# Optimization experiments

Hardware: AMD Instinct MI355X
Metric: run time of the kernel (lower is better)

Reference implementation:

```python
import jax, jax.numpy as jnp
import numpy as np
import math

HEADS = 8
HID = 32
MODES = 8
IN_CH = 4
SEQ = 32
B = 2
H = 64
W = 64


def spectral_conv(x, wr, wi):
    # x: [N, Cin, H, W]; w: [Cin, Cout, m, m] complex (low rfft2 modes only)
    n, _, h, w = x.shape
    m = wr.shape[2]
    xf = jnp.fft.rfft2(x)  # [N, Cin, H, W//2+1] complex64
    of = jnp.einsum('bixy,ioxy->boxy', xf[:, :, :m, :m], wr + 1j * wi)
    out_ft = jnp.zeros((n, wr.shape[1], h, w // 2 + 1), dtype=of.dtype)
    out_ft = out_ft.at[:, :, :m, :m].set(of)
    return jnp.fft.irfft2(out_ft, s=(h, w))


def conv1x1(x, w, b):
    # x: [N, Cin, H, W], w: [Cout, Cin], b: [Cout]
    return jnp.einsum('bchw,oc->bohw', x, w) + b[None, :, None, None]


def setup_inputs() -> dict:
    key = jax.random.key(0)
    ks = jax.random.split(key, 16)
    hd = HEADS * HID
    s = 0.02
    inp = {
        'v': jax.random.normal(ks[0], (B, SEQ, IN_CH, H, W), dtype=jnp.float32),
        'qwr': jax.random.normal(ks[1], (IN_CH, hd, MODES, MODES), dtype=jnp.float32) * s,
        'qwi': jax.random.normal(ks[2], (IN_CH, hd, MODES, MODES), dtype=jnp.float32) * s,
        'kwr': jax.random.normal(ks[3], (IN_CH, hd, MODES, MODES), dtype=jnp.float32) * s,
        'kwi': jax.random.normal(ks[4], (IN_CH, hd, MODES, MODES), dtype=jnp.float32) * s,
        'vwr': jax.random.normal(ks[5], (IN_CH, hd, MODES, MODES), dtype=jnp.float32) * s,
        'vwi': jax.random.normal(ks[6], (IN_CH, hd, MODES, MODES), dtype=jnp.float32) * s,
        'u1wr': jax.random.normal(ks[7], (hd, HID, MODES, MODES), dtype=jnp.float32) * s,
        'u1wi': jax.random.normal(ks[8], (hd, HID, MODES, MODES), dtype=jnp.float32) * s,
        'u2wr': jax.random.normal(ks[9], (HID, IN_CH, MODES, MODES), dtype=jnp.float32) * s,
        'u2wi': jax.random.normal(ks[10], (HID, IN_CH, MODES, MODES), dtype=jnp.float32) * s,
        's1w': jax.random.normal(ks[11], (HID, hd), dtype=jnp.float32) * s,
        's1b': jnp.zeros((HID,), dtype=jnp.float32),
        's2w': jax.random.normal(ks[12], (IN_CH, HID), dtype=jnp.float32) * s,
        's2b': jnp.zeros((IN_CH,), dtype=jnp.float32),
    }
    return inp


def reference(v, qwr, qwi, kwr, kwi, vwr, vwi, u1wr, u1wi, u2wr, u2wi, s1w, s1b, s2w, s2b):
    b, s, c, h, w = v.shape
    scale = 1.0 / math.sqrt(HID / HEADS)
    vr = v.reshape(b * s, c, h, w)
    embed = (b, HEADS, s, -1, h, w)  # same raw row-major reshape as torch
    q = spectral_conv(vr, qwr, qwi).reshape(embed)
    k = spectral_conv(vr, kwr, kwi).reshape(embed)
    val = spectral_conv(vr, vwr, vwi).reshape(embed)
    # inner products over channel dim, then dx^2-weighted spatial integral
    ip = jnp.einsum('bhsdrc,bhtdrc->bhstrc', q, k) * scale
    dx = 1.0 / h
    l2 = jnp.sum(ip, axis=(-2, -1)) * (dx * dx)  # [b, h, s1, s2]
    A = jax.nn.softmax(l2, axis=-1)
    u = jnp.einsum('bhst,bhtdrc->bhsdrc', A, val)
    u = jnp.transpose(u, (0, 2, 1, 3, 4, 5)).reshape(b * s, HEADS * u.shape[3], h, w)
    # SimpleFNO: gelu(conv1) + skip1, then conv2 + skip2
    x1 = jax.nn.gelu(spectral_conv(u, u1wr, u1wi), approximate=False) + conv1x1(u, s1w, s1b)
    x2 = spectral_conv(x1, u2wr, u2wi) + conv1x1(x1, s2w, s2b)
    return x2.reshape(b, s, c, h, w)
```

## Files before the change

kernel.cpp:

```cpp
#include <hip/hip_runtime.h>
#include <math.h>

#define HEADS 8
#define HIDC  32
#define MODES 8
#define IN_CH 4
#define SEQ   32
#define NS    64
#define HD    256
#define NM    64
#define NPIX  4096
#define TWO_PI_D 6.283185307179586476925286766559

__device__ __forceinline__ float2 f2(float a, float b){ return make_float2(a,b); }

__global__ void twiddle_kernel(float2* __restrict__ Etab){
  int t = threadIdx.x;
  int a = t >> 3, b = t & 7;
  double sv, cv; sincos(TWO_PI_D * ((a*b) & 63) / 64.0, &sv, &cv);
  Etab[t] = f2((float)cv, (float)sv);
}

__global__ __launch_bounds__(512) void fwd_dft_kernel(const float* __restrict__ src,
                                                      const float2* __restrict__ Etab,
                                                      float2* __restrict__ dst){
  int f = blockIdx.x, tid = threadIdx.x;
  __shared__ float  s_fld[64*68];
  __shared__ float2 s_e[64][8];
  __shared__ float2 s_a1[64][8];
  if (tid < 512) ((float2*)s_e)[tid] = Etab[tid];
  const float4* f4 = (const float4*)(src + (size_t)f*NPIX);
  for (int k = tid; k < 1024; k += 512){
    float4 v = f4[k];
    int y = k >> 4, x4 = (k & 15)*4;
    float* row = &s_fld[y*68 + x4];
    row[0]=v.x; row[1]=v.y; row[2]=v.z; row[3]=v.w;
  }
  __syncthreads();
  {
    int o = tid;
    int y = o >> 3, kx = o & 7;
    const float4* row = (const float4*)&s_fld[y*68];
    float sr = 0.f, si = 0.f;
    for (int x4 = 0; x4 < 16; ++x4){
      float4 v = row[x4];
      int xb = x4*4;
      float2 c0 = s_e[xb+0][kx], c1 = s_e[xb+1][kx];
      float2 c2 = s_e[xb+2][kx], c3 = s_e[xb+3][kx];
      sr += v.x*c0.x + v.y*c1.x + v.z*c2.x + v.w*c3.x;
      si -= v.x*c0.y + v.y*c1.y + v.z*c2.y + v.w*c3.y;
    }
    s_a1[y][kx] = f2(sr, si);
  }
  __syncthreads();
  if (tid < 64){
    int ky = tid >> 3, kx = tid & 7;
    float sr = 0.f, si = 0.f;
    for (int y = 0; y < 64; ++y){
      float2 a = s_a1[y][kx];
      float2 cs = s_e[y][ky];
      sr += a.x*cs.x + a.y*cs.y;
      si += a.y*cs.x - a.x*cs.y;
    }
    dst[(size_t)f*NM + tid] = f2(sr, si);
  }
}

__global__ __launch_bounds__(256) void gram_kernel(const float* __restrict__ qwr, const float* __restrict__ qwi,
                                                   const float* __restrict__ kwr, const float* __restrict__ kwi,
                                                   float2* __restrict__ G2, float* __restrict__ Gdc){
  int m = blockIdx.x, tid = threadIdx.x;
  __shared__ float qsr[4][257], qsi[4][257], ksr[4][257], ksi[4][257];
  for (int k = tid; k < 1024; k += 256){
    int i = k >> 8, c = k & 255;
    size_t a = ((size_t)(i*256 + c))*64 + m;
    qsr[i][c] = qwr[a]; qsi[i][c] = qwi[a];
    ksr[i][c] = kwr[a]; ksi[i][c] = kwi[a];
  }
  __syncthreads();
  int kx = m & 7, ky = m >> 3;
  float w = (kx >= 1) ? 2.0f : ((ky >= 1) ? 0.5f : 0.0f);
  for (int e = tid; e < 1024; e += 256){
    int P = e >> 7, T = (e >> 4) & 7, i = (e >> 2) & 3, j = e & 3;
    float grr=0.f, gri=0.f, gir=0.f, gii=0.f;
    for (int d = 0; d < 32; ++d){
      float ar = qsr[i][P*32+d], ai = qsi[i][P*32+d];
      float br = ksr[j][T*32+d], bi = ksi[j][T*32+d];
      grr += ar*br; gri += ar*bi; gir += ai*br; gii += ai*bi;
    }
    G2[(size_t)(((m*8+P)*4+i)*4+j)*8 + T] = f2(w*(grr+gii), w*(gir-gri));
    if (m == 0){
      int o = ((P*4+i)*4+j)*8 + T;
      Gdc[o] = grr; Gdc[1024+o] = gri; Gdc[2048+o] = gir; Gdc[3072+o] = gii;
    }
  }
}

__global__ __launch_bounds__(256) void attn_kernel(const float2* __restrict__ Vf,
                                                   const float2* __restrict__ G2,
                                                   const float* __restrict__ Gdc,
                                                   float* __restrict__ A){
  int bx = blockIdx.x;
  int s = bx & 31;
  int base = ((bx >> 8) * 32) + (((bx >> 5) & 7) * 4);
  int tid = threadIdx.x;
  int t = tid & 31, mc = tid >> 5;
  __shared__ float2 s_vf[4][IN_CH][64];
  __shared__ float  s_part[8][33];
  for (int k = tid; k < 4*IN_CH*64; k += 256){
    int m = k & 63, c = (k>>6)&3, smp = k>>8;
    s_vf[smp][c][m] = Vf[((size_t)(base+smp)*IN_CH + c)*NM + m];
  }
  __syncthreads();
  int sg = s >> 3, P = s & 7;
  int tg = t >> 3, T = t & 7;
  float acc = 0.f;
  for (int mm = 0; mm < 8; ++mm){
    int m = mc*8 + mm;
    const float2* g = G2 + (size_t)((m*8+P)*16)*8 + T;
    float sub = 0.f;
    for (int i = 0; i < 4; ++i){
      float2 a = s_vf[sg][i][m];
      for (int j = 0; j < 4; ++j){
        float2 b = s_vf[tg][j][m];
        float zr = a.x*b.x + a.y*b.y;
        float zi = a.y*b.x - a.x*b.y;
        float2 gv = g[(size_t)(i*4+j)*8];
        sub += zr*gv.x - zi*gv.y;
      }
    }
    acc += sub;
  }
  if (mc == 0){
    float sub = 0.f;
    for (int i = 0; i < 4; ++i){
      float2 a = s_vf[sg][i][0];
      for (int j = 0; j < 4; ++j){
        float2 b = s_vf[tg][j][0];
        int o = ((P*4+i)*4+j)*8 + T;
        sub += a.x*b.x*Gdc[o] - a.x*b.y*Gdc[1024+o]
             - a.y*b.x*Gdc[2048+o] + a.y*b.y*Gdc[3072+o];
      }
    }
    acc += sub;
  }
  s_part[mc][t] = acc;
  __syncthreads();
  if (tid < 32){
    float l2 = 0.f;
    for (int k = 0; k < 8; ++k) l2 += s_part[k][tid];
    l2 *= 0.5f / (4096.0f * 4096.0f);
    float mx = l2;
    for (int off = 16; off; off >>= 1) mx = fmaxf(mx, __shfl_xor(mx, off, 32));
    float e = expf(l2 - mx);
    float sm = e;
    for (int off = 16; off; off >>= 1) sm += __shfl_xor(sm, off, 32);
    A[(size_t)bx*32 + tid] = e / sm;
  }
}

__global__ __launch_bounds__(256) void v1t_kernel(const float* __restrict__ vwr,
                                                  const float* __restrict__ vwi,
                                                  float2* __restrict__ vwT){
  int t = blockIdx.x*256 + threadIdx.x;
  int m = t & 63, r = t >> 6, i = r >> 8, c = r & 255;
  vwT[((size_t)m*256 + c)*4 + i] = f2(vwr[t], vwi[t]);
}

__global__ __launch_bounds__(256) void uspec_kernel(const float2* __restrict__ Vf,
                                                    const float2* __restrict__ vwT,
                                                    const float* __restrict__ A,
                                                    float2* __restrict__ Uf){
  int bid = blockIdx.x;
  int mg = bid & 31, hh = (bid >> 5) & 7, b = bid >> 8;
  int m0 = mg*2;
  int nbase = b*32 + hh*4;
  int tid = threadIdx.x;
  __shared__ float2 s_vw[4][2][256];
  __shared__ float2 s_vv[4][2][256];
  __shared__ float  s_A[32][33];
  __shared__ float2 s_vf[4][4][2];
  for (int k = tid; k < 2048; k += 256){
    int mm = k >> 10, c = (k >> 2) & 255, i = k & 3;
    s_vw[i][mm][c] = vwT[(size_t)m0*1024 + k];
  }
  for (int k = tid; k < 1024; k += 256)
    s_A[k>>5][k&31] = A[(size_t)((b*8+hh)*32 + (k>>5))*32 + (k&31)];
  if (tid < 32){
    int smp = tid >> 3, i = (tid >> 1) & 3, mm = tid & 1;
    s_vf[smp][i][mm] = Vf[((size_t)(nbase+smp)*4 + i)*64 + m0 + mm];
  }
  __syncthreads();
  for (int k = tid; k < 2048; k += 256){
    int smp = k >> 9, mm = (k >> 8) & 1, c = k & 255;
    float sr = 0.f, si = 0.f;
    for (int i = 0; i < 4; ++i){
      float2 v = s_vf[smp][i][mm];
      float2 w = s_vw[i][mm][c];
      sr += v.x*w.x - v.y*w.y;
      si += v.x*w.y + v.y*w.x;
    }
    s_vv[smp][mm][c] = f2(sr, si);
  }
  __syncthreads();
  int sg = tid >> 5, d = tid & 31;
  float2 acc[4][2];
  for (int ss = 0; ss < 4; ++ss)
    for (int mm = 0; mm < 2; ++mm) acc[ss][mm] = f2(0.f, 0.f);
  for (int tt = 0; tt < 32; ++tt){
    int tg = tt >> 3, c = (tt & 7)*32 + d;
    float a0 = s_A[sg*4+0][tt], a1 = s_A[sg*4+1][tt];
    float a2 = s_A[sg*4+2][tt], a3 = s_A[sg*4+3][tt];
    for (int mm = 0; mm < 2; ++mm){
      float2 v = s_vv[tg][mm][c];
      acc[0][mm].x += a0*v.x; acc[0][mm].y += a0*v.y;
      acc[1][mm].x += a1*v.x; acc[1][mm].y += a1*v.y;
      acc[2][mm].x += a2*v.x; acc[2][mm].y += a2*v.y;
      acc[3][mm].x += a3*v.x; acc[3][mm].y += a3*v.y;
    }
  }
  for (int ss = 0; ss < 4; ++ss){
    int n = b*32 + sg*4 + ss;
    for (int mm = 0; mm < 2; ++mm)
      Uf[((size_t)n*64 + m0 + mm)*256 + hh*32 + d] = acc[ss][mm];
  }
}

__global__ __launch_bounds__(256) void u1t_kernel(const float* __restrict__ u1wr,
                                                  const float* __restrict__ u1wi,
                                                  float4* __restrict__ u1wT){
  int t = blockIdx.x*256 + threadIdx.x;
  int m = t & 63, r = t >> 6, c = r >> 5, o1 = r & 31;
  float pr = ((m & 7)==0 && m) ? 0.5f : 1.0f;
  float pi = m ? pr : 0.0f;
  float wr = u1wr[t], wi = u1wi[t];
  u1wT[((size_t)m*256 + c)*32 + o1] = make_float4(pr*wr, pi*wi, pr*wi, pi*wr);
}

__global__ __launch_bounds__(128) void mix1_kernel(const float2* __restrict__ Uf,
                                                   const float4* __restrict__ u1wT,
                                                   const float* __restrict__ s1w,
                                                   float2* __restrict__ U1f, float2* __restrict__ S1f){
  int bid = blockIdx.x;
  int n0 = (bid >> 4)*4, mg = bid & 15, m0 = mg*4;
  int tid = threadIdx.x;
  __shared__ float2 s_u[4][4][256];
  for (int k = tid; k < 4096; k += 128){
    int smp = k >> 10, mm = (k >> 8) & 3, c = k & 255;
    s_u[smp][mm][c] = Uf[((size_t)(n0+smp)*64 + m0 + mm)*256 + c];
  }
  __syncthreads();
  int o1 = tid & 31, mm = tid >> 5;
  int m = m0 + mm;
  const float4* wp = u1wT + (size_t)m*8192 + o1;
  const float* swp = s1w + o1*256;
  float2 au[4], asv[4];
  #pragma unroll
  for (int s = 0; s < 4; ++s){ au[s] = f2(0.f,0.f); asv[s] = f2(0.f,0.f); }
  for (int c = 0; c < 256; ++c){
    float4 w = wp[(size_t)c*32];
    float sw = swp[c];
    #pragma unroll
    for (int s = 0; s < 4; ++s){
      float2 u = s_u[s][mm][c];
      au[s].x  += u.x*w.x - u.y*w.y;
      au[s].y  += u.x*w.z + u.y*w.w;
      asv[s].x += u.x*sw;
      asv[s].y += u.y*sw;
    }
  }
  #pragma unroll
  for (int s = 0; s < 4; ++s){
    size_t ob = ((size_t)(n0+s)*32 + o1)*64 + m;
    U1f[ob] = au[s]; S1f[ob] = asv[s];
  }
}

__global__ __launch_bounds__(256) void xg_kernel(const float2* __restrict__ Etab,
                                                 const float2* __restrict__ U1f,
                                                 float2* __restrict__ Xg){
  int f0 = blockIdx.x*2, tid = threadIdx.x;
  __shared__ float2 s_e[64][8];
  __shared__ float2 s_gu[2][64];
  __shared__ float2 s_tu[2][64][8];
  __shared__ float  s_fld[2][64*68];
  for (int e = tid; e < 512; e += 256) ((float2*)s_e)[e] = Etab[e];
  if (tid < 128) ((float2*)s_gu)[tid] = U1f[(size_t)f0*NM + tid];
  __syncthreads();
  for (int o = tid; o < 1024; o += 256){
    int fl = o >> 9, r = o & 511, y = r >> 3, kx = r & 7;
    float wf = (kx ? 2.0f : 1.0f) * (1.0f/4096.0f);
    float ar=0.f, ai=0.f;
    for (int ky = 0; ky < 8; ++ky){
      float2 cs = s_e[y][ky];
      float2 gu = s_gu[fl][ky*8+kx];
      ar += gu.x*cs.x - gu.y*cs.y;
      ai += gu.x*cs.y + gu.y*cs.x;
    }
    s_tu[fl][y][kx] = f2(ar*wf, ai*wf);
  }
  __syncthreads();
  int xx = tid & 63;
  float2 ce[8];
  #pragma unroll
  for (int k = 0; k < 8; ++k) ce[k] = s_e[xx][k];
  #pragma unroll 2
  for (int i = 0; i < 16; ++i){
    int p = i*256 + tid, y = p >> 6;
    const float4* tp0 = (const float4*)&s_tu[0][y][0];
    const float4* tp1 = (const float4*)&s_tu[1][y][0];
    float4 a0=tp0[0], a1=tp0[1], a2=tp0[2], a3=tp0[3];
    float4 b0=tp1[0], b1=tp1[1], b2=tp1[2], b3=tp1[3];
    float v0 = a0.x*ce[0].x - a0.y*ce[0].y + a0.z*ce[1].x - a0.w*ce[1].y
             + a1.x*ce[2].x - a1.y*ce[2].y + a1.z*ce[3].x - a1.w*ce[3].y
             + a2.x*ce[4].x - a2.y*ce[4].y + a2.z*ce[5].x - a2.w*ce[5].y
             + a3.x*ce[6].x - a3.y*ce[6].y + a3.z*ce[7].x - a3.w*ce[7].y;
    float v1 = b0.x*ce[0].x - b0.y*ce[0].y + b0.z*ce[1].x - b0.w*ce[1].y
             + b1.x*ce[2].x - b1.y*ce[2].y + b1.z*ce[3].x - b1.w*ce[3].y
             + b2.x*ce[4].x - b2.y*ce[4].y + b2.z*ce[5].x - b2.w*ce[5].y
             + b3.x*ce[6].x - b3.y*ce[6].y + b3.z*ce[7].x - b3.w*ce[7].y;
    float g0 = 0.5f * v0 * (1.0f + erff(v0 * 0.70710678f));
    float g1 = 0.5f * v1 * (1.0f + erff(v1 * 0.70710678f));
    s_fld[0][y*68 + xx] = g0;
    s_fld[1][y*68 + xx] = g1;
  }
  __syncthreads();
  float2 (*s_a1)[64][8] = s_tu;
  for (int o = tid; o < 1024; o += 256){
    int fl = o >> 9, r = o & 511, y = r >> 3, kx = r & 7;
    const float4* row = (const float4*)&s_fld[fl][y*68];
    float sr = 0.f, si = 0.f;
    for (int x4 = 0; x4 < 16; ++x4){
      float4 v = row[x4];
      int xb = x4*4;
      float2 c0 = s_e[xb+0][kx], c1 = s_e[xb+1][kx];
      float2 c2 = s_e[xb+2][kx], c3 = s_e[xb+3][kx];
      sr += v.x*c0.x + v.y*c1.x + v.z*c2.x + v.w*c3.x;
      si -= v.x*c0.y + v.y*c1.y + v.z*c2.y + v.w*c3.y;
    }
    s_a1[fl][y][kx] = f2(sr, si);
  }
  __syncthreads();
  if (tid < 128){
    int fl = tid >> 6, t6 = tid & 63;
    int ky = t6 >> 3, kx = t6 & 7;
    float sr = 0.f, si = 0.f;
    for (int y = 0; y < 64; ++y){
      float2 a = s_a1[fl][y][kx];
      float2 cs = s_e[y][ky];
      sr += a.x*cs.x + a.y*cs.y;
      si += a.y*cs.x - a.x*cs.y;
    }
    Xg[(size_t)(f0+fl)*NM + t6] = f2(sr, si);
  }
}

__global__ __launch_bounds__(256) void final_kernel(const float2* __restrict__ Etab,
                                                    const float2* __restrict__ U1f,
                                                    const float2* __restrict__ S1f,
                                                    const float2* __restrict__ Xg,
                                                    const float* __restrict__ u2wr, const float* __restrict__ u2wi,
                                                    const float* __restrict__ s1b,
                                                    const float* __restrict__ s2w, const float* __restrict__ s2b,
                                                    float* __restrict__ out){
  int n = blockIdx.x >> 4, tile = blockIdx.x & 15, y0 = tile*4;
  int tid = threadIdx.x;
  __shared__ float2 s_e[64][8];
  __shared__ float2 s_u1[32][64];
  __shared__ float2 s_T[32][4][8];
  __shared__ float2 s_os[4][64];
  __shared__ float2 s_tmp[4][4][8];
  __shared__ float  s_w2[128], s_s1b[32], s_b2[4];
  for (int e = tid; e < 512; e += 256) ((float2*)s_e)[e] = Etab[e];
  for (int k = tid; k < 2048; k += 256) ((float2*)s_u1)[k] = U1f[(size_t)n*2048 + k];
  if (tid < 128) s_w2[tid] = s2w[tid];
  else if (tid < 160) s_s1b[tid-128] = s1b[tid-128];
  else if (tid < 164) s_b2[tid-160] = s2b[tid-160];
  __syncthreads();
  for (int e = tid; e < 1024; e += 256){
    int c = e >> 5, yy = (e >> 3) & 3, kx = e & 7;
    int y = y0 + yy;
    float wf = (kx ? 2.0f : 1.0f) * (1.0f/4096.0f);
    float ar = 0.f, ai = 0.f;
    for (int ky = 0; ky < 8; ++ky){
      float2 cs = s_e[y][ky];
      float2 g = s_u1[c][ky*8+kx];
      ar += g.x*cs.x - g.y*cs.y;
      ai += g.x*cs.y + g.y*cs.x;
    }
    s_T[c][yy][kx] = f2(ar*wf, ai*wf);
  }
  {
    int o2 = tid >> 6, m = tid & 63;
    float prm = ((m & 7)==0 && m) ? 0.5f : 1.0f;
    float pim = m ? prm : 0.0f;
    float dc = (m == 0) ? 4096.0f : 0.0f;
    float cr = 0.f, ci = 0.f;
    for (int o1 = 0; o1 < 32; ++o1){
      float2 xg = Xg[((size_t)n*32 + o1)*NM + m];
      float2 sf = S1f[((size_t)n*32 + o1)*NM + m];
      float Xr = xg.x + sf.x*prm + dc*s_s1b[o1];
      float Xi = xg.y + sf.y*pim;
      size_t wb = ((size_t)(o1*IN_CH + o2))*NM + m;
      float wr = u2wr[wb], wi = u2wi[wb];
      float sw = s_w2[o2*32 + o1];
      cr += Xr*wr - Xi*wi + sw*sf.x;
      ci += Xr*wi + Xi*wr + sw*sf.y;
    }
    s_os[o2][m] = f2(cr, ci);
  }
  __syncthreads();
  if (tid < 128){
    int o2 = tid >> 5, yy = (tid >> 3) & 3, kx = tid & 7;
    int y = y0 + yy;
    float wf = (kx ? 2.0f : 1.0f) * (1.0f/4096.0f);
    float tr=0.f, ti=0.f;
    for (int ky = 0; ky < 8; ++ky){
      float2 cs = s_e[y][ky];
      float2 g = s_os[o2][ky*8+kx];
      tr += g.x*cs.x - g.y*cs.y;
      ti += g.x*cs.y + g.y*cs.x;
    }
    s_tmp[o2][yy][kx] = f2(tr*wf, ti*wf);
  }
  __syncthreads();
  int yy = tid >> 6, xx = tid & 63;
  float2 ce[8];
  #pragma unroll
  for (int k = 0; k < 8; ++k) ce[k] = s_e[xx][k];
  float a0 = s_b2[0], a1 = s_b2[1], a2 = s_b2[2], a3 = s_b2[3];
  for (int c = 0; c < 32; ++c){
    float b = s_s1b[c];
    a0 += s_w2[c]*b; a1 += s_w2[32+c]*b; a2 += s_w2[64+c]*b; a3 += s_w2[96+c]*b;
  }
  for (int c = 0; c < 32; ++c){
    const float4* tp = (const float4*)&s_T[c][yy][0];
    float4 t0 = tp[0], t1 = tp[1], t2 = tp[2], t3 = tp[3];
    float vu = t0.x*ce[0].x - t0.y*ce[0].y + t0.z*ce[1].x - t0.w*ce[1].y
             + t1.x*ce[2].x - t1.y*ce[2].y + t1.z*ce[3].x - t1.w*ce[3].y
             + t2.x*ce[4].x - t2.y*ce[4].y + t2.z*ce[5].x - t2.w*ce[5].y
             + t3.x*ce[6].x - t3.y*ce[6].y + t3.z*ce[7].x - t3.w*ce[7].y;
    float g = 0.5f * vu * (1.0f + erff(vu * 0.70710678f));
    a0 += s_w2[c]*g; a1 += s_w2[32+c]*g; a2 += s_w2[64+c]*g; a3 += s_w2[96+c]*g;
  }
  float sp[4];
  #pragma unroll
  for (int o2 = 0; o2 < 4; ++o2){
    const float4* tp = (const float4*)&s_tmp[o2][yy][0];
    float4 t0 = tp[0], t1 = tp[1], t2 = tp[2], t3 = tp[3];
    sp[o2] = t0.x*ce[0].x - t0.y*ce[0].y + t0.z*ce[1].x - t0.w*ce[1].y
           + t1.x*ce[2].x - t1.y*ce[2].y + t1.z*ce[3].x - t1.w*ce[3].y
           + t2.x*ce[4].x - t2.y*ce[4].y + t2.z*ce[5].x - t2.w*ce[5].y
           + t3.x*ce[6].x - t3.y*ce[6].y + t3.z*ce[7].x - t3.w*ce[7].y;
  }
  int p = (y0 + yy)*64 + xx;
  float* ob = out + (size_t)n*IN_CH*NPIX;
  ob[p]          = a0 + sp[0];
  ob[NPIX + p]   = a1 + sp[1];
  ob[2*NPIX + p] = a2 + sp[2];
  ob[3*NPIX + p] = a3 + sp[3];
}

extern "C" void kernel_launch(void* const* d_in, const int* in_sizes, int n_in,
                              void* d_out, int out_size, void* d_ws, size_t ws_size,
                              hipStream_t stream) {
  (void)in_sizes; (void)n_in; (void)out_size; (void)ws_size;
  const float* v    = (const float*)d_in[0];
  const float* qwr  = (const float*)d_in[1];
  const float* qwi  = (const float*)d_in[2];
  const float* kwr  = (const float*)d_in[3];
  const float* kwi  = (const float*)d_in[4];
  const float* vwr  = (const float*)d_in[5];
  const float* vwi  = (const float*)d_in[6];
  const float* u1wr = (const float*)d_in[7];
  const float* u1wi = (const float*)d_in[8];
  const float* u2wr = (const float*)d_in[9];
  const float* u2wi = (const float*)d_in[10];
  const float* s1w  = (const float*)d_in[11];
  const float* s1b  = (const float*)d_in[12];
  const float* s2w  = (const float*)d_in[13];
  const float* s2b  = (const float*)d_in[14];
  float* out = (float*)d_out;

  float* ws = (float*)d_ws;
  size_t off = 0;
  float2* Etab =(float2*)(ws + off); off += 1024;
  float2* Vf   = (float2*)(ws + off); off += (size_t)NS*IN_CH*NM*2;
  float2* G2   = (float2*)(ws + off); off += (size_t)65536*2;
  float*  Gdc  =          (ws + off); off += 4096;
  float*  A    =          (ws + off); off += 16384;
  float2* Uf   = (float2*)(ws + off); off += (size_t)NS*NM*HD*2;
  float2* U1f  = (float2*)(ws + off); off += (size_t)NS*HIDC*NM*2;
  float2* S1f  = (float2*)(ws + off); off += (size_t)NS*HIDC*NM*2;
  float2* Xg   = (float2*)(ws + off); off += (size_t)NS*HIDC*NM*2;
  float4* u1wT = (float4*)(ws + off); off += (size_t)524288*4;
  float2* vwT  = (float2*)(ws + off); off += (size_t)65536*2;

  twiddle_kernel<<<1, 512, 0, stream>>>(Etab);
  fwd_dft_kernel<<<NS*IN_CH, 512, 0, stream>>>(v, Etab, Vf);
  gram_kernel<<<64, 256, 0, stream>>>(qwr, qwi, kwr, kwi, G2, Gdc);
  u1t_kernel<<<2048, 256, 0, stream>>>(u1wr, u1wi, u1wT);
  v1t_kernel<<<256, 256, 0, stream>>>(vwr, vwi, vwT);
  attn_kernel<<<512, 256, 0, stream>>>(Vf, G2, Gdc, A);
  uspec_kernel<<<512, 256, 0, stream>>>(Vf, vwT, A, Uf);
  mix1_kernel<<<256, 128, 0, stream>>>(Uf, u1wT, s1w, U1f, S1f);
  xg_kernel<<<1024, 256, 0, stream>>>(Etab, U1f, Xg);
  final_kernel<<<NS*16, 256, 0, stream>>>(Etab, U1f, S1f, Xg, u2wr, u2wi, s1b, s2w, s2b, out);
}
```

Measured before the change: 240.4 us.

## Split accumulator chains, retile mix1, widen xg blocks, add transposed twiddle table

Reduction loops in the forward DFT, xg and final kernels are split into two independent accumulator chains to shorten FMA dependency latency. mix1 is retiled to 8 samples by 2 modes with 256 threads and stages s1w in shared memory instead of reading it from global memory. xg now runs 512 threads per block, and xg and final read the x-direction twiddles from a transposed shared table to avoid strided LDS reads. The changes cost more shared memory and registers, which may reduce occupancy, and the split sums slightly change floating-point rounding.

```diff
diff --git a/kernel.cpp b/kernel.cpp
--- a/kernel.cpp
+++ b/kernel.cpp
@@ -38,31 +38,44 @@
   }
   __syncthreads();
   {
-    int o = tid;
-    int y = o >> 3, kx = o & 7;
+    int y = tid >> 3, kx = tid & 7;
     const float4* row = (const float4*)&s_fld[y*68];
-    float sr = 0.f, si = 0.f;
-    for (int x4 = 0; x4 < 16; ++x4){
+    float sr0=0.f, si0=0.f, sr1=0.f, si1=0.f;
+    for (int x4 = 0; x4 < 8; ++x4){
       float4 v = row[x4];
       int xb = x4*4;
       float2 c0 = s_e[xb+0][kx], c1 = s_e[xb+1][kx];
       float2 c2 = s_e[xb+2][kx], c3 = s_e[xb+3][kx];
-      sr += v.x*c0.x + v.y*c1.x + v.z*c2.x + v.w*c3.x;
-      si -= v.x*c0.y + v.y*c1.y + v.z*c2.y + v.w*c3.y;
-    }
-    s_a1[y][kx] = f2(sr, si);
+      sr0 += v.x*c0.x + v.y*c1.x + v.z*c2.x + v.w*c3.x;
+      si0 -= v.x*c0.y + v.y*c1.y + v.z*c2.y + v.w*c3.y;
+    }
+    for (int x4 = 8; x4 < 16; ++x4){
+      float4 v = row[x4];
+      int xb = x4*4;
+      float2 c0 = s_e[xb+0][kx], c1 = s_e[xb+1][kx];
+      float2 c2 = s_e[xb+2][kx], c3 = s_e[xb+3][kx];
+      sr1 += v.x*c0.x + v.y*c1.x + v.z*c2.x + v.w*c3.x;
+      si1 -= v.x*c0.y + v.y*c1.y + v.z*c2.y + v.w*c3.y;
+    }
+    s_a1[y][kx] = f2(sr0+sr1, si0+si1);
   }
   __syncthreads();
   if (tid < 64){
     int ky = tid >> 3, kx = tid & 7;
-    float sr = 0.f, si = 0.f;
-    for (int y = 0; y < 64; ++y){
+    float sr0=0.f, si0=0.f, sr1=0.f, si1=0.f;
+    for (int y = 0; y < 32; ++y){
       float2 a = s_a1[y][kx];
       float2 cs = s_e[y][ky];
-      sr += a.x*cs.x + a.y*cs.y;
-      si += a.y*cs.x - a.x*cs.y;
-    }
-    dst[(size_t)f*NM + tid] = f2(sr, si);
+      sr0 += a.x*cs.x + a.y*cs.y;
+      si0 += a.y*cs.x - a.x*cs.y;
+    }
+    for (int y = 32; y < 64; ++y){
+      float2 a = s_a1[y][kx];
+      float2 cs = s_e[y][ky];
+      sr1 += a.x*cs.x + a.y*cs.y;
+      si1 += a.y*cs.x - a.x*cs.y;
+    }
+    dst[(size_t)f*NM + tid] = f2(sr0+sr1, si0+si1);
   }
 }
 
@@ -237,121 +250,146 @@
   u1wT[((size_t)m*256 + c)*32 + o1] = make_float4(pr*wr, pi*wi, pr*wi, pi*wr);
 }
 
-__global__ __launch_bounds__(128) void mix1_kernel(const float2* __restrict__ Uf,
+__global__ __launch_bounds__(256) void mix1_kernel(const float2* __restrict__ Uf,
                                                    const float4* __restrict__ u1wT,
                                                    const float* __restrict__ s1w,
                                                    float2* __restrict__ U1f, float2* __restrict__ S1f){
   int bid = blockIdx.x;
-  int n0 = (bid >> 4)*4, mg = bid & 15, m0 = mg*4;
+  int mg = bid & 31, n0 = (bid >> 5)*8, m0 = mg*2;
   int tid = threadIdx.x;
-  __shared__ float2 s_u[4][4][256];
-  for (int k = tid; k < 4096; k += 128){
-    int smp = k >> 10, mm = (k >> 8) & 3, c = k & 255;
-    s_u[smp][mm][c] = Uf[((size_t)(n0+smp)*64 + m0 + mm)*256 + c];
-  }
-  __syncthreads();
-  int o1 = tid & 31, mm = tid >> 5;
-  int m = m0 + mm;
+  __shared__ float2 s_u[8][2][256];
+  __shared__ float  s_w1[32][257];
+  for (int it = 0; it < 16; ++it){
+    int s = it >> 1, mm = it & 1;
+    s_u[s][mm][tid] = Uf[((size_t)(n0+s)*64 + m0 + mm)*256 + tid];
+  }
+  for (int k = tid; k < 8192; k += 256)
+    s_w1[k>>8][k&255] = s1w[k];
+  __syncthreads();
+  int o1 = tid & 31, mm = (tid >> 5) & 1, sh = tid >> 6;
+  int m = m0 + mm, sA = sh*2, sB = sh*2+1;
   const float4* wp = u1wT + (size_t)m*8192 + o1;
-  const float* swp = s1w + o1*256;
-  float2 au[4], asv[4];
-  #pragma unroll
-  for (int s = 0; s < 4; ++s){ au[s] = f2(0.f,0.f); asv[s] = f2(0.f,0.f); }
+  float2 au0 = f2(0,0), au1 = f2(0,0), as0 = f2(0,0), as1 = f2(0,0);
+  #pragma unroll 4
   for (int c = 0; c < 256; ++c){
     float4 w = wp[(size_t)c*32];
-    float sw = swp[c];
-    #pragma unroll
-    for (int s = 0; s < 4; ++s){
-      float2 u = s_u[s][mm][c];
-      au[s].x  += u.x*w.x - u.y*w.y;
-      au[s].y  += u.x*w.z + u.y*w.w;
-      asv[s].x += u.x*sw;
-      asv[s].y += u.y*sw;
-    }
-  }
-  #pragma unroll
-  for (int s = 0; s < 4; ++s){
-    size_t ob = ((size_t)(n0+s)*32 + o1)*64 + m;
-    U1f[ob] = au[s]; S1f[ob] = asv[s];
-  }
-}
-
-__global__ __launch_bounds__(256) void xg_kernel(const float2* __restrict__ Etab,
+    float sw = s_w1[o1][c];
+    float2 uA = s_u[sA][mm][c];
+    float2 uB = s_u[sB][mm][c];
+    au0.x += uA.x*w.x - uA.y*w.y;  au0.y += uA.x*w.z + uA.y*w.w;
+    au1.x += uB.x*w.x - uB.y*w.y;  au1.y += uB.x*w.z + uB.y*w.w;
+    as0.x += uA.x*sw;  as0.y += uA.y*sw;
+    as1.x += uB.x*sw;  as1.y += uB.y*sw;
+  }
+  size_t obA = ((size_t)(n0+sA)*32 + o1)*64 + m;
+  size_t obB = ((size_t)(n0+sB)*32 + o1)*64 + m;
+  U1f[obA] = au0; S1f[obA] = as0;
+  U1f[obB] = au1; S1f[obB] = as1;
+}
+
+__global__ __launch_bounds__(512) void xg_kernel(const float2* __restrict__ Etab,
                                                  const float2* __restrict__ U1f,
                                                  float2* __restrict__ Xg){
   int f0 = blockIdx.x*2, tid = threadIdx.x;
   __shared__ float2 s_e[64][8];
+  __shared__ float2 s_eT[8][64];
   __shared__ float2 s_gu[2][64];
   __shared__ float2 s_tu[2][64][8];
   __shared__ float  s_fld[2][64*68];
-  for (int e = tid; e < 512; e += 256) ((float2*)s_e)[e] = Etab[e];
+  if (tid < 512){
+    float2 v = Etab[tid];
+    int a = tid >> 3, b = tid & 7;
+    s_e[a][b] = v; s_eT[b][a] = v;
+  }
   if (tid < 128) ((float2*)s_gu)[tid] = U1f[(size_t)f0*NM + tid];
   __syncthreads();
-  for (int o = tid; o < 1024; o += 256){
+  for (int o = tid; o < 1024; o += 512){
     int fl = o >> 9, r = o & 511, y = r >> 3, kx = r & 7;
     float wf = (kx ? 2.0f : 1.0f) * (1.0f/4096.0f);
-    float ar=0.f, ai=0.f;
-    for (int ky = 0; ky < 8; ++ky){
+    float a0=0.f, b0=0.f, a1=0.f, b1=0.f;
+    for (int ky = 0; ky < 4; ++ky){
       float2 cs = s_e[y][ky];
       float2 gu = s_gu[fl][ky*8+kx];
-      ar += gu.x*cs.x - gu.y*cs.y;
-      ai += gu.x*cs.y + gu.y*cs.x;
-    }
-    s_tu[fl][y][kx] = f2(ar*wf, ai*wf);
+      a0 += gu.x*cs.x - gu.y*cs.y;
+      b0 += gu.x*cs.y + gu.y*cs.x;
+    }
+    for (int ky = 4; ky < 8; ++ky){
+      float2 cs = s_e[y][ky];
+      float2 gu = s_gu[fl][ky*8+kx];
+      a1 += gu.x*cs.x - gu.y*cs.y;
+      b1 += gu.x*cs.y + gu.y*cs.x;
+    }
+    s_tu[fl][y][kx] = f2((a0+a1)*wf, (b0+b1)*wf);
   }
   __syncthreads();
   int xx = tid & 63;
   float2 ce[8];
   #pragma unroll
-  for (int k = 0; k < 8; ++k) ce[k] = s_e[xx][k];
-  #pragma unroll 2
-  for (int i = 0; i < 16; ++i){
-    int p = i*256 + tid, y = p >> 6;
+  for (int k = 0; k < 8; ++k) ce[k] = s_eT[k][xx];
+  for (int i = 0; i < 8; ++i){
+    int p = i*512 + tid, y = p >> 6;
     const float4* tp0 = (const float4*)&s_tu[0][y][0];
     const float4* tp1 = (const float4*)&s_tu[1][y][0];
     float4 a0=tp0[0], a1=tp0[1], a2=tp0[2], a3=tp0[3];
     float4 b0=tp1[0], b1=tp1[1], b2=tp1[2], b3=tp1[3];
-    float v0 = a0.x*ce[0].x - a0.y*ce[0].y + a0.z*ce[1].x - a0.w*ce[1].y
-             + a1.x*ce[2].x - a1.y*ce[2].y + a1.z*ce[3].x - a1.w*ce[3].y
-             + a2.x*ce[4].x - a2.y*ce[4].y + a2.z*ce[5].x - a2.w*ce[5].y
+    float h0 = a0.x*ce[0].x - a0.y*ce[0].y + a0.z*ce[1].x - a0.w*ce[1].y
+             + a1.x*ce[2].x - a1.y*ce[2].y + a1.z*ce[3].x - a1.w*ce[3].y;
+    float h1 = a2.x*ce[4].x - a2.y*ce[4].y + a2.z*ce[5].x - a2.w*ce[5].y
              + a3.x*ce[6].x - a3.y*ce[6].y + a3.z*ce[7].x - a3.w*ce[7].y;
-    float v1 = b0.x*ce[0].x - b0.y*ce[0].y + b0.z*ce[1].x - b0.w*ce[1].y
-             + b1.x*ce[2].x - b1.y*ce[2].y + b1.z*ce[3].x - b1.w*ce[3].y
-             + b2.x*ce[4].x - b2.y*ce[4].y + b2.z*ce[5].x - b2.w*ce[5].y
+    float g0 = a0.x*0.f;
+    float k0 = b0.x*ce[0].x - b0.y*ce[0].y + b0.z*ce[1].x - b0.w*ce[1].y
+             + b1.x*ce[2].x - b1.y*ce[2].y + b1.z*ce[3].x - b1.w*ce[3].y;
+    float k1 = b2.x*ce[4].x - b2.y*ce[4].y + b2.z*ce[5].x - b2.w*ce[5].y
              + b3.x*ce[6].x - b3.y*ce[6].y + b3.z*ce[7].x - b3.w*ce[7].y;
-    float g0 = 0.5f * v0 * (1.0f + erff(v0 * 0.70710678f));
-    float g1 = 0.5f * v1 * (1.0f + erff(v1 * 0.70710678f));
-    s_fld[0][y*68 + xx] = g0;
-    s_fld[1][y*68 + xx] = g1;
+    float v0 = h0 + h1, v1 = k0 + k1;
+    float ga = 0.5f * v0 * (1.0f + erff(v0 * 0.70710678f));
+    float gb = 0.5f * v1 * (1.0f + erff(v1 * 0.70710678f));
+    (void)g0;
+    s_fld[0][y*68 + xx] = ga;
+    s_fld[1][y*68 + xx] = gb;
   }
   __syncthreads();
   float2 (*s_a1)[64][8] = s_tu;
-  for (int o = tid; o < 1024; o += 256){
+  for (int o = tid; o < 1024; o += 512){
     int fl = o >> 9, r = o & 511, y = r >> 3, kx = r & 7;
     const float4* row = (const float4*)&s_fld[fl][y*68];
-    float sr = 0.f, si = 0.f;
-    for (int x4 = 0; x4 < 16; ++x4){
+    float sr0=0.f, si0=0.f, sr1=0.f, si1=0.f;
+    for (int x4 = 0; x4 < 8; ++x4){
       float4 v = row[x4];
       int xb = x4*4;
       float2 c0 = s_e[xb+0][kx], c1 = s_e[xb+1][kx];
       float2 c2 = s_e[xb+2][kx], c3 = s_e[xb+3][kx];
-      sr += v.x*c0.x + v.y*c1.x + v.z*c2.x + v.w*c3.x;
-      si -= v.x*c0.y + v.y*c1.y + v.z*c2.y + v.w*c3.y;
-    }
-    s_a1[fl][y][kx] = f2(sr, si);
+      sr0 += v.x*c0.x + v.y*c1.x + v.z*c2.x + v.w*c3.x;
+      si0 -= v.x*c0.y + v.y*c1.y + v.z*c2.y + v.w*c3.y;
+    }
+    for (int x4 = 8; x4 < 16; ++x4){
+      float4 v = row[x4];
+      int xb = x4*4;
+      float2 c0 = s_e[xb+0][kx], c1 = s_e[xb+1][kx];
+      float2 c2 = s_e[xb+2][kx], c3 = s_e[xb+3][kx];
+      sr1 += v.x*c0.x + v.y*c1.x + v.z*c2.x + v.w*c3.x;
+      si1 -= v.x*c0.y + v.y*c1.y + v.z*c2.y + v.w*c3.y;
+    }
+    s_a1[fl][y][kx] = f2(sr0+sr1, si0+si1);
   }
   __syncthreads();
   if (tid < 128){
     int fl = tid >> 6, t6 = tid & 63;
     int ky = t6 >> 3, kx = t6 & 7;
-    float sr = 0.f, si = 0.f;
-    for (int y = 0; y < 64; ++y){
+    float sr0=0.f, si0=0.f, sr1=0.f, si1=0.f;
+    for (int y = 0; y < 32; ++y){
       float2 a = s_a1[fl][y][kx];
       float2 cs = s_e[y][ky];
-      sr += a.x*cs.x + a.y*cs.y;
-      si += a.y*cs.x - a.x*cs.y;
-    }
-    Xg[(size_t)(f0+fl)*NM + t6] = f2(sr, si);
+      sr0 += a.x*cs.x + a.y*cs.y;
+      si0 += a.y*cs.x - a.x*cs.y;
+    }
+    for (int y = 32; y < 64; ++y){
+      float2 a = s_a1[fl][y][kx];
+      float2 cs = s_e[y][ky];
+      sr1 += a.x*cs.x + a.y*cs.y;
+      si1 += a.y*cs.x - a.x*cs.y;
+    }
+    Xg[(size_t)(f0+fl)*NM + t6] = f2(sr0+sr1, si0+si1);
   }
 }
 
@@ -366,12 +404,16 @@
   int n = blockIdx.x >> 4, tile = blockIdx.x & 15, y0 = tile*4;
   int tid = threadIdx.x;
   __shared__ float2 s_e[64][8];
+  __shared__ float2 s_eT[8][64];
   __shared__ float2 s_u1[32][64];
   __shared__ float2 s_T[32][4][8];
   __shared__ float2 s_os[4][64];
   __shared__ float2 s_tmp[4][4][8];
   __shared__ float  s_w2[128], s_s1b[32], s_b2[4];
-  for (int e = tid; e < 512; e += 256) ((float2*)s_e)[e] = Etab[e];
+  for (int e = tid; e < 512; e += 256){
+    float2 v = Etab[e];
+    s_e[e>>3][e&7] = v; s_eT[e&7][e>>3] = v;
+  }
   for (int k = tid; k < 2048; k += 256) ((float2*)s_u1)[k] = U1f[(size_t)n*2048 + k];
   if (tid < 128) s_w2[tid] = s2w[tid];
   else if (tid < 160) s_s1b[tid-128] = s1b[tid-128];
@@ -427,7 +469,7 @@
   int yy = tid >> 6, xx = tid & 63;
   float2 ce[8];
   #pragma unroll
-  for (int k = 0; k < 8; ++k) ce[k] = s_e[xx][k];
+  for (int k = 0; k < 8; ++k) ce[k] = s_eT[k][xx];
   float a0 = s_b2[0], a1 = s_b2[1], a2 = s_b2[2], a3 = s_b2[3];
   for (int c = 0; c < 32; ++c){
     float b = s_s1b[c];
@@ -436,10 +478,11 @@
   for (int c = 0; c < 32; ++c){
     const float4* tp = (const float4*)&s_T[c][yy][0];
     float4 t0 = tp[0], t1 = tp[1], t2 = tp[2], t3 = tp[3];
-    float vu = t0.x*ce[0].x - t0.y*ce[0].y + t0.z*ce[1].x - t0.w*ce[1].y
-             + t1.x*ce[2].x - t1.y*ce[2].y + t1.z*ce[3].x - t1.w*ce[3].y
-             + t2.x*ce[4].x - t2.y*ce[4].y + t2.z*ce[5].x - t2.w*ce[5].y
+    float h0 = t0.x*ce[0].x - t0.y*ce[0].y + t0.z*ce[1].x - t0.w*ce[1].y
+             + t1.x*ce[2].x - t1.y*ce[2].y + t1.z*ce[3].x - t1.w*ce[3].y;
+    float h1 = t2.x*ce[4].x - t2.y*ce[4].y + t2.z*ce[5].x - t2.w*ce[5].y
              + t3.x*ce[6].x - t3.y*ce[6].y + t3.z*ce[7].x - t3.w*ce[7].y;
+    float vu = h0 + h1;
     float g = 0.5f * vu * (1.0f + erff(vu * 0.70710678f));
     a0 += s_w2[c]*g; a1 += s_w2[32+c]*g; a2 += s_w2[64+c]*g; a3 += s_w2[96+c]*g;
   }
@@ -448,10 +491,11 @@
   for (int o2 = 0; o2 < 4; ++o2){
     const float4* tp = (const float4*)&s_tmp[o2][yy][0];
     float4 t0 = tp[0], t1 = tp[1], t2 = tp[2], t3 = tp[3];
-    sp[o2] = t0.x*ce[0].x - t0.y*ce[0].y + t0.z*ce[1].x - t0.w*ce[1].y
-           + t1.x*ce[2].x - t1.y*ce[2].y + t1.z*ce[3].x - t1.w*ce[3].y
-           + t2.x*ce[4].x - t2.y*ce[4].y + t2.z*ce[5].x - t2.w*ce[5].y
-           + t3.x*ce[6].x - t3.y*ce[6].y + t3.z*ce[7].x - t3.w*ce[7].y;
+    float h0 = t0.x*ce[0].x - t0.y*ce[0].y + t0.z*ce[1].x - t0.w*ce[1].y
+             + t1.x*ce[2].x - t1.y*ce[2].y + t1.z*ce[3].x - t1.w*ce[3].y;
+    float h1 = t2.x*ce[4].x - t2.y*ce[4].y + t2.z*ce[5].x - t2.w*ce[5].y
+             + t3.x*ce[6].x - t3.y*ce[6].y + t3.z*ce[7].x - t3.w*ce[7].y;
+    sp[o2] = h0 + h1;
   }
   int p = (y0 + yy)*64 + xx;
   float* ob = out + (size_t)n*IN_CH*NPIX;
@@ -503,7 +547,7 @@
   v1t_kernel<<<256, 256, 0, stream>>>(vwr, vwi, vwT);
   attn_kernel<<<512, 256, 0, stream>>>(Vf, G2, Gdc, A);
   uspec_kernel<<<512, 256, 0, stream>>>(Vf, vwT, A, Uf);
-  mix1_kernel<<<256, 128, 0, stream>>>(Uf, u1wT, s1w, U1f, S1f);
-  xg_kernel<<<1024, 256, 0, stream>>>(Etab, U1f, Xg);
+  mix1_kernel<<<256, 256, 0, stream>>>(Uf, u1wT, s1w, U1f, S1f);
+  xg_kernel<<<1024, 512, 0, stream>>>(Etab, U1f, Xg);
   final_kernel<<<NS*16, 256, 0, stream>>>(Etab, U1f, S1f, Xg, u2wr, u2wi, s1b, s2w, s2b, out);
 }
```

New measurement: 233.2 us. 1.03x faster.
